# Performance work log

Measured on AMD Instinct MI355X. Metric: run time of the kernel, lower is better.

Reference implementation:

```python
import jax, jax.numpy as jnp
import numpy as np


def setup_inputs() -> dict:
    key = jax.random.key(0)
    k1, k2, k3, k4 = jax.random.split(key, 4)
    B, N, DIN, DOUT = 4, 4096, 512, 64
    x = jax.random.normal(k1, (B, N, DIN), dtype=jnp.float32)
    Wq = jax.random.normal(k2, (DIN, DOUT), dtype=jnp.float32) * (1.0 / np.sqrt(DIN))
    Wk = jax.random.normal(k3, (DIN, DOUT), dtype=jnp.float32) * (1.0 / np.sqrt(DIN))
    Wv = jax.random.normal(k4, (DIN, DOUT), dtype=jnp.float32) * (1.0 / np.sqrt(DIN))
    return {"x": x, "Wq": Wq, "Wk": Wk, "Wv": Wv}


def reference(x, Wq, Wk, Wv):
    # x: [B, N, Din]; projections: [B, N, Dout]
    q = jnp.einsum('bnd,de->bne', x, Wq)
    k = jnp.einsum('bnd,de->bne', x, Wk)
    v = jnp.einsum('bnd,de->bne', x, Wv)
    N = x.shape[1]
    scale = 1.0 / jnp.sqrt(jnp.asarray(k.shape[-1], dtype=x.dtype))
    # scores: [B, N, N]; causal mask (strict upper triangle -> -inf)
    scores = jnp.einsum('bqe,bke->bqk', q, k)
    causal = jnp.tril(jnp.ones((N, N), dtype=bool))  # True where allowed
    scores = jnp.where(causal[None], scores, -jnp.inf)
    att = jax.nn.softmax(scores * scale, axis=-1)
    # dropout p=0.0 -> identity (eval-mode equivalent)
    return jnp.einsum('bqk,bke->bqe', att, v)
```

## Files before the change

kernel.cpp:

```cpp
#include <hip/hip_runtime.h>
#include <hip/hip_bf16.h>

#define BB 4
#define NN 4096
#define DIN 512
#define DD 64

typedef __attribute__((ext_vector_type(8))) short short8;
typedef __attribute__((ext_vector_type(4))) float f32x4;
typedef __attribute__((ext_vector_type(4))) unsigned short us4;
typedef __attribute__((ext_vector_type(2))) unsigned int u32x2;
using bf16 = __hip_bfloat16;

#define QSCALE 0.18033688011112042f

__device__ inline void mfma_16x16x32(f32x4& d, short8 a, short8 b) {
    asm("v_mfma_f32_16x16x32_bf16 %0, %1, %2, %0" : "+v"(d) : "v"(a), "v"(b));
}

__device__ inline unsigned cvt_pk_bf16(float lo, float hi) {
    unsigned r;
    asm("v_cvt_pk_bf16_f32 %0, %1, %2" : "=v"(r) : "v"(lo), "v"(hi));
    return r;
}

__device__ inline short8 load_cvt8(const float* __restrict__ src) {
    f32x4 f0 = *(const f32x4*)(src);
    f32x4 f1 = *(const f32x4*)(src + 4);
    bf16 t[8];
    #pragma unroll
    for (int j = 0; j < 4; ++j) t[j]     = __float2bfloat16(f0[j]);
    #pragma unroll
    for (int j = 0; j < 4; ++j) t[4 + j] = __float2bfloat16(f1[j]);
    return *(short8*)t;
}

__host__ __device__ inline int pfx(int qt, int cl) {
    int K = 2 << cl;
    int n = qt + K;
    int a = n >> (cl + 1);
    int r = n - (a << (cl + 1));
    return a * (a - 1) * (K >> 1) + r * a;
}

__global__ __launch_bounds__(256) void convw_kernel(
    const float* __restrict__ Wq, const float* __restrict__ Wk,
    const float* __restrict__ Wv, bf16* __restrict__ WT)
{
    int idx = blockIdx.x * 256 + threadIdx.x;
    int w   = idx >> 15;
    int rem = idx & 32767;
    int n   = rem >> 9;
    int kk  = rem & 511;
    const float* W = (w == 0) ? Wq : (w == 1) ? Wk : Wv;
    WT[idx] = __float2bfloat16(W[kk * DD + n]);
}

__global__ __launch_bounds__(256) void proj_kernel(
    const float* __restrict__ x, const bf16* __restrict__ WT,
    bf16* __restrict__ q, bf16* __restrict__ k, bf16* __restrict__ vT)
{
    __shared__ __align__(16) char xs[65536];
    const int tid   = threadIdx.x;
    const int row0  = blockIdx.x * 64;
    const int b     = row0 >> 12;
    const int nrow0 = row0 & 4095;

    const float* xb = x + (size_t)row0 * DIN;
    #pragma unroll
    for (int i = 0; i < 16; ++i) {
        int c   = tid + i * 256;
        int row = c >> 6;
        int cc  = c & 63;
        const float* src = xb + row * DIN + cc * 8;
        int off = row * 1024 + ((cc * 16) ^ ((row & 7) << 4));
        *(short8*)(xs + off) = load_cvt8(src);
    }
    __syncthreads();

    const int lane  = tid & 63;
    const int l16   = lane & 15;
    const int lg    = lane >> 4;
    const int wave  = tid >> 6;
    const int cbase = wave * 48;

    f32x4 acc[4][3];
    #pragma unroll
    for (int rt = 0; rt < 4; ++rt)
        #pragma unroll
        for (int ct = 0; ct < 3; ++ct) acc[rt][ct] = (f32x4){0.f, 0.f, 0.f, 0.f};

    const bf16* wb = WT + (size_t)(cbase + l16) * DIN + lg * 8;

    #pragma unroll 2
    for (int ks = 0; ks < 16; ++ks) {
        short8 a[4], bfr[3];
        #pragma unroll
        for (int rt = 0; rt < 4; ++rt) {
            int row = rt * 16 + l16;
            a[rt] = *(const short8*)(xs + row * 1024 +
                                     ((ks * 64 + lg * 16) ^ ((row & 7) << 4)));
        }
        #pragma unroll
        for (int ct = 0; ct < 3; ++ct)
            bfr[ct] = *(const short8*)(wb + ct * 16 * DIN + ks * 32);
        #pragma unroll
        for (int rt = 0; rt < 4; ++rt)
            #pragma unroll
            for (int ct = 0; ct < 3; ++ct)
                mfma_16x16x32(acc[rt][ct], a[rt], bfr[ct]);
    }

    #pragma unroll
    for (int ct = 0; ct < 3; ++ct) {
        int g = cbase + ct * 16 + l16;
        int w = g >> 6;
        int n = g & 63;
        #pragma unroll
        for (int rt = 0; rt < 4; ++rt) {
            if (w == 2) {
                us4 pv;
                #pragma unroll
                for (int r = 0; r < 4; ++r) {
                    bf16 hv = __float2bfloat16(acc[rt][ct][r]);
                    pv[r] = *(unsigned short*)&hv;
                }
                *(us4*)(vT + ((size_t)b * DD + n) * NN + nrow0 + rt * 16 + lg * 4) = pv;
            } else {
                bf16* dst = (w == 0) ? q : k;
                float sc  = (w == 0) ? QSCALE : 1.0f;
                #pragma unroll
                for (int r = 0; r < 4; ++r) {
                    int row = nrow0 + rt * 16 + lg * 4 + r;
                    dst[((size_t)b * NN + row) * DD + n] =
                        __float2bfloat16(acc[rt][ct][r] * sc);
                }
            }
        }
    }
}

__global__ __launch_bounds__(256) void attn_split_kernel(
    const bf16* __restrict__ q, const bf16* __restrict__ k,
    const bf16* __restrict__ vT,
    unsigned short* __restrict__ partO, float* __restrict__ partML,
    float* __restrict__ out, int cl)
{
    const int perB = pfx(64, cl);
    const int wblk = blockIdx.x;
    const int b    = wblk / perB;
    const int u    = wblk - b * perB;
    int lo = 0, hi = 63;
    while (lo < hi) {
        int mid = (lo + hi + 1) >> 1;
        if (pfx(mid, cl) <= u) lo = mid; else hi = mid - 1;
    }
    const int qt = lo;
    const int s  = u - pfx(qt, cl);
    const size_t sidx = (size_t)wblk;

    const int T  = (qt + 2) >> 1;
    const int t0 = s << cl;
    int t1 = t0 + (1 << cl); if (t1 > T) t1 = T;
    const int K2 = 2 << cl;
    const int U  = (qt + K2) >> (cl + 1);

    const int wave = threadIdx.x >> 6;
    const int lane = threadIdx.x & 63;
    const int l16  = lane & 15;
    const int lg   = lane >> 4;

    __shared__ __align__(16) char klds[16384];
    __shared__ __align__(16) char vlds[16384];
    __shared__ __align__(16) char plds[4][4096];
    char* pbl = plds[wave];
    const int swz = (l16 & 7) << 4;

    const int row0g = qt * 64 + wave * 16;
    const int qrow  = row0g + l16;

    const bf16* qbase = q + ((size_t)b * NN + row0g + l16) * DD + lg * 8;
    short8 qfrag0 = *(const short8*)(qbase);
    short8 qfrag1 = *(const short8*)(qbase + 32);

    f32x4 oacc[4];
    #pragma unroll
    for (int dt = 0; dt < 4; ++dt) oacc[dt] = (f32x4){0.f, 0.f, 0.f, 0.f};
    float m = -INFINITY, l = 0.f;

    const char* kglob = (const char*)(k  + (size_t)b * NN * DD);
    const char* vglob = (const char*)(vT + (size_t)b * DD * NN);
    short8 kst[4], vst[4];
    int k_wr[4], v_wr[4], v_dd[4];
    #pragma unroll
    for (int i = 0; i < 4; ++i) {
        int L = wave * 4096 + i * 1024 + lane * 16;
        k_wr[i] = L ^ (((L >> 7) & 7) << 4);
        int dd = wave * 16 + i * 4 + (lane >> 4);
        v_dd[i] = dd;
        v_wr[i] = dd * 256 + (((lane & 15) * 16) ^ ((dd & 7) << 4));
    }

    {
        const char* kt = kglob + (size_t)t0 * 16384;
        const char* vt = vglob + (size_t)t0 * 256;
        #pragma unroll
        for (int i = 0; i < 4; ++i)
            kst[i] = *(const short8*)(kt + wave * 4096 + i * 1024 + lane * 16);
        #pragma unroll
        for (int i = 0; i < 4; ++i)
            vst[i] = *(const short8*)(vt + (size_t)v_dd[i] * 8192 + (lane & 15) * 16);
        #pragma unroll
        for (int i = 0; i < 4; ++i) *(short8*)(klds + k_wr[i]) = kst[i];
        #pragma unroll
        for (int i = 0; i < 4; ++i) *(short8*)(vlds + v_wr[i]) = vst[i];
    }
    __syncthreads();

    #pragma unroll 1
    for (int t = t0; t < t1; ++t) {
        f32x4 sc[8];
        #pragma unroll
        for (int ct = 0; ct < 8; ++ct) sc[ct] = (f32x4){0.f, 0.f, 0.f, 0.f};
        __builtin_amdgcn_s_setprio(1);
        #pragma unroll
        for (int ct = 0; ct < 8; ++ct) {
            short8 kf0 = *(const short8*)(klds + (ct * 16 + l16) * 128 + ((lg * 16) ^ swz));
            short8 kf1 = *(const short8*)(klds + (ct * 16 + l16) * 128 + ((64 + lg * 16) ^ swz));
            mfma_16x16x32(sc[ct], kf0, qfrag0);
            mfma_16x16x32(sc[ct], kf1, qfrag1);
        }
        __builtin_amdgcn_s_setprio(0);

        if (t + 1 < t1) {
            const char* kt = kglob + (size_t)(t + 1) * 16384;
            const char* vt = vglob + (size_t)(t + 1) * 256;
            #pragma unroll
            for (int i = 0; i < 4; ++i)
                kst[i] = *(const short8*)(kt + wave * 4096 + i * 1024 + lane * 16);
            #pragma unroll
            for (int i = 0; i < 4; ++i)
                vst[i] = *(const short8*)(vt + (size_t)v_dd[i] * 8192 + (lane & 15) * 16);
        }

        if (t * 128 + 127 > row0g) {
            #pragma unroll
            for (int ct = 0; ct < 8; ++ct) {
                int gk = t * 128 + ct * 16 + lg * 4;
                #pragma unroll
                for (int r = 0; r < 4; ++r)
                    if (gk + r > qrow)
                        sc[ct][r] = -INFINITY;
            }
        }

        float m4[8];
        #pragma unroll
        for (int ct = 0; ct < 8; ++ct)
            m4[ct] = fmaxf(fmaxf(sc[ct][0], sc[ct][1]), fmaxf(sc[ct][2], sc[ct][3]));
        float mt = fmaxf(fmaxf(fmaxf(m4[0], m4[1]), fmaxf(m4[2], m4[3])),
                         fmaxf(fmaxf(m4[4], m4[5]), fmaxf(m4[6], m4[7])));
        mt = fmaxf(mt, __shfl_xor(mt, 16));
        mt = fmaxf(mt, __shfl_xor(mt, 32));

        float mn    = fmaxf(m, mt);
        float alpha = exp2f(m - mn);
        m = mn;

        float s4[8];
        #pragma unroll
        for (int ct = 0; ct < 8; ++ct) {
            float p0 = exp2f(sc[ct][0] - m);
            float p1 = exp2f(sc[ct][1] - m);
            float p2 = exp2f(sc[ct][2] - m);
            float p3 = exp2f(sc[ct][3] - m);
            sc[ct][0] = p0; sc[ct][1] = p1; sc[ct][2] = p2; sc[ct][3] = p3;
            s4[ct] = (p0 + p1) + (p2 + p3);
        }
        float ls = ((s4[0] + s4[1]) + (s4[2] + s4[3])) +
                   ((s4[4] + s4[5]) + (s4[6] + s4[7]));
        ls += __shfl_xor(ls, 16);
        ls += __shfl_xor(ls, 32);
        l = l * alpha + ls;

        float ar[4];
        #pragma unroll
        for (int r = 0; r < 4; ++r) ar[r] = __shfl(alpha, lg * 4 + r);
        #pragma unroll
        for (int dt = 0; dt < 4; ++dt)
            #pragma unroll
            for (int r = 0; r < 4; ++r)
                oacc[dt][r] *= ar[r];

        #pragma unroll
        for (int ct = 0; ct < 8; ++ct) {
            u32x2 pw = (u32x2){cvt_pk_bf16(sc[ct][0], sc[ct][1]),
                               cvt_pk_bf16(sc[ct][2], sc[ct][3])};
            *(u32x2*)(pbl + l16 * 256 + ((ct * 32 + lg * 8) ^ swz)) = pw;
        }
        asm volatile("s_waitcnt lgkmcnt(0)" ::: "memory");
        short8 pa[4];
        #pragma unroll
        for (int kc = 0; kc < 4; ++kc)
            pa[kc] = *(const short8*)(pbl + l16 * 256 + ((kc * 64 + lg * 16) ^ swz));

        __builtin_amdgcn_s_setprio(1);
        #pragma unroll
        for (int dt = 0; dt < 4; ++dt) {
            #pragma unroll
            for (int kc = 0; kc < 4; ++kc) {
                short8 vf = *(const short8*)(vlds + (dt * 16 + l16) * 256 +
                                             ((kc * 64 + lg * 16) ^ swz));
                mfma_16x16x32(oacc[dt], pa[kc], vf);
            }
        }
        __builtin_amdgcn_s_setprio(0);

        if (t + 1 < t1) {
            __syncthreads();
            #pragma unroll
            for (int i = 0; i < 4; ++i) *(short8*)(klds + k_wr[i]) = kst[i];
            #pragma unroll
            for (int i = 0; i < 4; ++i) *(short8*)(vlds + v_wr[i]) = vst[i];
            __syncthreads();
        }
    }

    if (U == 1) {
        float lr[4];
        #pragma unroll
        for (int r = 0; r < 4; ++r) lr[r] = __shfl(l, lg * 4 + r);
        #pragma unroll
        for (int dt = 0; dt < 4; ++dt) {
            #pragma unroll
            for (int r = 0; r < 4; ++r) {
                int row = row0g + lg * 4 + r;
                out[((size_t)b * NN + row) * DD + dt * 16 + l16] =
                    oacc[dt][r] / lr[r];
            }
        }
        return;
    }

    {
        unsigned short hv[16];
        #pragma unroll
        for (int dt = 0; dt < 4; ++dt)
            #pragma unroll
            for (int r = 0; r < 4; ++r) {
                bf16 h = __float2bfloat16(oacc[dt][r]);
                hv[dt * 4 + r] = *(unsigned short*)&h;
            }
        unsigned short* dst = partO + sidx * 4096 + wave * 1024 + lane * 16;
        *(short8*)(dst)     = *(short8*)(hv);
        *(short8*)(dst + 8) = *(short8*)(hv + 8);
    }
    if (lg == 0) {
        partML[sidx * 128 + wave * 16 + l16]      = m;
        partML[sidx * 128 + 64 + wave * 16 + l16] = l;
    }
}

__global__ __launch_bounds__(256) void combine_kernel(
    const unsigned short* __restrict__ partO, const float* __restrict__ partML,
    float* __restrict__ out, int cl)
{
    const int blk2 = blockIdx.x;
    const int half = blk2 & 1;
    const int blk  = blk2 >> 1;
    const int qt   = blk & 63;
    const int b    = blk >> 6;

    const int K2 = 2 << cl;
    const int U  = (qt + K2) >> (cl + 1);
    if (U == 1) return;

    const int tid  = threadIdx.x;
    const int w    = tid >> 6;
    const int lane = tid & 63;
    const int l16  = lane & 15;
    const int lg   = lane >> 4;

    const int perB = pfx(64, cl);
    const size_t base = (size_t)b * perB + pfx(qt, cl);

    float M[4] = {-INFINITY, -INFINITY, -INFINITY, -INFINITY};
    for (int s = 0; s < U; ++s)
        #pragma unroll
        for (int r = 0; r < 4; ++r)
            M[r] = fmaxf(M[r], partML[(base + s) * 128 + w * 16 + lg * 4 + r]);

    float L[4] = {0.f, 0.f, 0.f, 0.f};
    float acc[8];
    #pragma unroll
    for (int i = 0; i < 8; ++i) acc[i] = 0.f;

    for (int s = 0; s < U; ++s) {
        float e[4];
        #pragma unroll
        for (int r = 0; r < 4; ++r) {
            float ms = partML[(base + s) * 128 + w * 16 + lg * 4 + r];
            e[r] = exp2f(ms - M[r]);
            L[r] += partML[(base + s) * 128 + 64 + w * 16 + lg * 4 + r] * e[r];
        }
        short8 v = *(const short8*)(partO + (base + s) * 4096 + w * 1024 +
                                    lane * 16 + half * 8);
        #pragma unroll
        for (int j = 0; j < 8; ++j) {
            unsigned fb = ((unsigned)(unsigned short)v[j]) << 16;
            acc[j] += *(float*)&fb * e[j & 3];
        }
    }
    #pragma unroll
    for (int j = 0; j < 8; ++j) {
        int reg = half * 8 + j;
        int row = qt * 64 + w * 16 + lg * 4 + (j & 3);
        int dd  = (reg >> 2) * 16 + l16;
        out[((size_t)b * NN + row) * DD + dd] = acc[j] / L[j & 3];
    }
}

extern "C" void kernel_launch(void* const* d_in, const int* in_sizes, int n_in,
                              void* d_out, int out_size, void* d_ws, size_t ws_size,
                              hipStream_t stream) {
    const float* x  = (const float*)d_in[0];
    const float* Wq = (const float*)d_in[1];
    const float* Wk = (const float*)d_in[2];
    const float* Wv = (const float*)d_in[3];

    bf16* q  = (bf16*)d_ws;
    bf16* k  = q  + (size_t)BB * NN * DD;
    bf16* vT = k  + (size_t)BB * NN * DD;
    bf16* WT = vT + (size_t)BB * NN * DD;
    char* pbase = (char*)(WT + 3 * DD * DIN);
    size_t mis = (size_t)pbase & 15;
    if (mis) pbase += 16 - mis;
    size_t fixed = (size_t)(pbase - (char*)d_ws);

    int cl = 2, perB = 0;
    for (; cl <= 3; ++cl) {
        perB = pfx(64, cl);
        size_t need = fixed + (size_t)BB * perB * (128 * 4 + 4096 * 2);
        if (need <= ws_size) break;
    }
    if (cl > 3) { cl = 3; perB = pfx(64, cl); }

    float* partML = (float*)pbase;
    unsigned short* partO = (unsigned short*)(partML + (size_t)BB * perB * 128);

    convw_kernel<<<(3 * DD * DIN) / 256, 256, 0, stream>>>(Wq, Wk, Wv, WT);
    proj_kernel<<<BB * NN / 64, 256, 0, stream>>>(x, WT, q, k, vT);
    attn_split_kernel<<<BB * perB, 256, 0, stream>>>(q, k, vT, partO, partML,
                                                     (float*)d_out, cl);
    combine_kernel<<<BB * 64 * 2, 256, 0, stream>>>(partO, partML, (float*)d_out, cl);
}
```

Before: 57.90 us.

## Halve attention key tile to 64 and rescale split-KV chunking

Shrinks the key/value tile in the split attention kernel from 128 to 64 keys, halving LDS buffers, staging registers and per-tile MFMA work, and rewrites the prefix/split arithmetic to match. The chunk-length exponent default rises from 2 to 3, so each split still spans up to 512 keys. The smaller tile lowers LDS and register use, which could raise occupancy and cuts masked work on diagonal tiles. The cost is twice as many loop iterations, with more barriers and softmax rescale steps per key.

```diff
diff --git a/kernel.cpp b/kernel.cpp
--- a/kernel.cpp
+++ b/kernel.cpp
@@ -36,11 +36,10 @@
 }
 
 __host__ __device__ inline int pfx(int qt, int cl) {
-    int K = 2 << cl;
-    int n = qt + K;
-    int a = n >> (cl + 1);
-    int r = n - (a << (cl + 1));
-    return a * (a - 1) * (K >> 1) + r * a;
+    int C = 1 << cl;
+    int a = qt >> cl;
+    int r = qt & (C - 1);
+    return C * a * (a + 1) / 2 + r * (a + 1);
 }
 
 __global__ __launch_bounds__(256) void convw_kernel(
@@ -159,20 +158,20 @@
     const int s  = u - pfx(qt, cl);
     const size_t sidx = (size_t)wblk;
 
-    const int T  = (qt + 2) >> 1;
+    const int C  = 1 << cl;
+    const int T  = qt + 1;
     const int t0 = s << cl;
-    int t1 = t0 + (1 << cl); if (t1 > T) t1 = T;
-    const int K2 = 2 << cl;
-    const int U  = (qt + K2) >> (cl + 1);
+    int t1 = t0 + C; if (t1 > T) t1 = T;
+    const int U  = (qt + C) >> cl;
 
     const int wave = threadIdx.x >> 6;
     const int lane = threadIdx.x & 63;
     const int l16  = lane & 15;
     const int lg   = lane >> 4;
 
-    __shared__ __align__(16) char klds[16384];
-    __shared__ __align__(16) char vlds[16384];
-    __shared__ __align__(16) char plds[4][4096];
+    __shared__ __align__(16) char klds[8192];
+    __shared__ __align__(16) char vlds[8192];
+    __shared__ __align__(16) char plds[4][2048];
     char* pbl = plds[wave];
     const int swz = (l16 & 7) << 4;
 
@@ -190,41 +189,41 @@
 
     const char* kglob = (const char*)(k  + (size_t)b * NN * DD);
     const char* vglob = (const char*)(vT + (size_t)b * DD * NN);
-    short8 kst[4], vst[4];
-    int k_wr[4], v_wr[4], v_dd[4];
-    #pragma unroll
-    for (int i = 0; i < 4; ++i) {
-        int L = wave * 4096 + i * 1024 + lane * 16;
-        k_wr[i] = L ^ (((L >> 7) & 7) << 4);
-        int dd = wave * 16 + i * 4 + (lane >> 4);
-        v_dd[i] = dd;
-        v_wr[i] = dd * 256 + (((lane & 15) * 16) ^ ((dd & 7) << 4));
+    short8 kst[2], vst[2];
+    int k_src[2], k_wr[2], v_src[2], v_wr[2];
+    #pragma unroll
+    for (int i = 0; i < 2; ++i) {
+        int L = threadIdx.x * 16 + i * 4096;
+        k_src[i] = L;
+        k_wr[i]  = L ^ (((L >> 7) & 7) << 4);
+        int dd    = L >> 7;
+        int inner = L & 127;
+        v_src[i] = dd * 8192 + inner;
+        v_wr[i]  = dd * 128 + (inner ^ ((dd & 7) << 4));
     }
 
     {
-        const char* kt = kglob + (size_t)t0 * 16384;
-        const char* vt = vglob + (size_t)t0 * 256;
-        #pragma unroll
-        for (int i = 0; i < 4; ++i)
-            kst[i] = *(const short8*)(kt + wave * 4096 + i * 1024 + lane * 16);
-        #pragma unroll
-        for (int i = 0; i < 4; ++i)
-            vst[i] = *(const short8*)(vt + (size_t)v_dd[i] * 8192 + (lane & 15) * 16);
-        #pragma unroll
-        for (int i = 0; i < 4; ++i) *(short8*)(klds + k_wr[i]) = kst[i];
-        #pragma unroll
-        for (int i = 0; i < 4; ++i) *(short8*)(vlds + v_wr[i]) = vst[i];
+        const char* kt = kglob + (size_t)t0 * 8192;
+        const char* vt = vglob + (size_t)t0 * 128;
+        #pragma unroll
+        for (int i = 0; i < 2; ++i) kst[i] = *(const short8*)(kt + k_src[i]);
+        #pragma unroll
+        for (int i = 0; i < 2; ++i) vst[i] = *(const short8*)(vt + v_src[i]);
+        #pragma unroll
+        for (int i = 0; i < 2; ++i) *(short8*)(klds + k_wr[i]) = kst[i];
+        #pragma unroll
+        for (int i = 0; i < 2; ++i) *(short8*)(vlds + v_wr[i]) = vst[i];
     }
     __syncthreads();
 
     #pragma unroll 1
     for (int t = t0; t < t1; ++t) {
-        f32x4 sc[8];
-        #pragma unroll
-        for (int ct = 0; ct < 8; ++ct) sc[ct] = (f32x4){0.f, 0.f, 0.f, 0.f};
+        f32x4 sc[4];
+        #pragma unroll
+        for (int ct = 0; ct < 4; ++ct) sc[ct] = (f32x4){0.f, 0.f, 0.f, 0.f};
         __builtin_amdgcn_s_setprio(1);
         #pragma unroll
-        for (int ct = 0; ct < 8; ++ct) {
+        for (int ct = 0; ct < 4; ++ct) {
             short8 kf0 = *(const short8*)(klds + (ct * 16 + l16) * 128 + ((lg * 16) ^ swz));
             short8 kf1 = *(const short8*)(klds + (ct * 16 + l16) * 128 + ((64 + lg * 16) ^ swz));
             mfma_16x16x32(sc[ct], kf0, qfrag0);
@@ -233,20 +232,18 @@
         __builtin_amdgcn_s_setprio(0);
 
         if (t + 1 < t1) {
-            const char* kt = kglob + (size_t)(t + 1) * 16384;
-            const char* vt = vglob + (size_t)(t + 1) * 256;
-            #pragma unroll
-            for (int i = 0; i < 4; ++i)
-                kst[i] = *(const short8*)(kt + wave * 4096 + i * 1024 + lane * 16);
-            #pragma unroll
-            for (int i = 0; i < 4; ++i)
-                vst[i] = *(const short8*)(vt + (size_t)v_dd[i] * 8192 + (lane & 15) * 16);
-        }
-
-        if (t * 128 + 127 > row0g) {
-            #pragma unroll
-            for (int ct = 0; ct < 8; ++ct) {
-                int gk = t * 128 + ct * 16 + lg * 4;
+            const char* kt = kglob + (size_t)(t + 1) * 8192;
+            const char* vt = vglob + (size_t)(t + 1) * 128;
+            #pragma unroll
+            for (int i = 0; i < 2; ++i) kst[i] = *(const short8*)(kt + k_src[i]);
+            #pragma unroll
+            for (int i = 0; i < 2; ++i) vst[i] = *(const short8*)(vt + v_src[i]);
+        }
+
+        if (t * 64 + 63 > row0g) {
+            #pragma unroll
+            for (int ct = 0; ct < 4; ++ct) {
+                int gk = t * 64 + ct * 16 + lg * 4;
                 #pragma unroll
                 for (int r = 0; r < 4; ++r)
                     if (gk + r > qrow)
@@ -254,12 +251,11 @@
             }
         }
 
-        float m4[8];
-        #pragma unroll
-        for (int ct = 0; ct < 8; ++ct)
+        float m4[4];
+        #pragma unroll
+        for (int ct = 0; ct < 4; ++ct)
             m4[ct] = fmaxf(fmaxf(sc[ct][0], sc[ct][1]), fmaxf(sc[ct][2], sc[ct][3]));
-        float mt = fmaxf(fmaxf(fmaxf(m4[0], m4[1]), fmaxf(m4[2], m4[3])),
-                         fmaxf(fmaxf(m4[4], m4[5]), fmaxf(m4[6], m4[7])));
+        float mt = fmaxf(fmaxf(m4[0], m4[1]), fmaxf(m4[2], m4[3]));
         mt = fmaxf(mt, __shfl_xor(mt, 16));
         mt = fmaxf(mt, __shfl_xor(mt, 32));
 
@@ -267,9 +263,9 @@
         float alpha = exp2f(m - mn);
         m = mn;
 
-        float s4[8];
-        #pragma unroll
-        for (int ct = 0; ct < 8; ++ct) {
+        float s4[4];
+        #pragma unroll
+        for (int ct = 0; ct < 4; ++ct) {
             float p0 = exp2f(sc[ct][0] - m);
             float p1 = exp2f(sc[ct][1] - m);
             float p2 = exp2f(sc[ct][2] - m);
@@ -277,8 +273,7 @@
             sc[ct][0] = p0; sc[ct][1] = p1; sc[ct][2] = p2; sc[ct][3] = p3;
             s4[ct] = (p0 + p1) + (p2 + p3);
         }
-        float ls = ((s4[0] + s4[1]) + (s4[2] + s4[3])) +
-                   ((s4[4] + s4[5]) + (s4[6] + s4[7]));
+        float ls = (s4[0] + s4[1]) + (s4[2] + s4[3]);
         ls += __shfl_xor(ls, 16);
         ls += __shfl_xor(ls, 32);
         l = l * alpha + ls;
@@ -293,35 +288,33 @@
                 oacc[dt][r] *= ar[r];
 
         #pragma unroll
-        for (int ct = 0; ct < 8; ++ct) {
+        for (int ct = 0; ct < 4; ++ct) {
             u32x2 pw = (u32x2){cvt_pk_bf16(sc[ct][0], sc[ct][1]),
                                cvt_pk_bf16(sc[ct][2], sc[ct][3])};
-            *(u32x2*)(pbl + l16 * 256 + ((ct * 32 + lg * 8) ^ swz)) = pw;
+            *(u32x2*)(pbl + l16 * 128 + ((ct * 32 + lg * 8) ^ swz)) = pw;
         }
         asm volatile("s_waitcnt lgkmcnt(0)" ::: "memory");
-        short8 pa[4];
-        #pragma unroll
-        for (int kc = 0; kc < 4; ++kc)
-            pa[kc] = *(const short8*)(pbl + l16 * 256 + ((kc * 64 + lg * 16) ^ swz));
+        short8 pa[2];
+        #pragma unroll
+        for (int kc = 0; kc < 2; ++kc)
+            pa[kc] = *(const short8*)(pbl + l16 * 128 + ((kc * 64 + lg * 16) ^ swz));
 
         __builtin_amdgcn_s_setprio(1);
         #pragma unroll
         for (int dt = 0; dt < 4; ++dt) {
-            #pragma unroll
-            for (int kc = 0; kc < 4; ++kc) {
-                short8 vf = *(const short8*)(vlds + (dt * 16 + l16) * 256 +
-                                             ((kc * 64 + lg * 16) ^ swz));
-                mfma_16x16x32(oacc[dt], pa[kc], vf);
-            }
+            short8 vf0 = *(const short8*)(vlds + (dt * 16 + l16) * 128 + ((lg * 16) ^ swz));
+            short8 vf1 = *(const short8*)(vlds + (dt * 16 + l16) * 128 + ((64 + lg * 16) ^ swz));
+            mfma_16x16x32(oacc[dt], pa[0], vf0);
+            mfma_16x16x32(oacc[dt], pa[1], vf1);
         }
         __builtin_amdgcn_s_setprio(0);
 
         if (t + 1 < t1) {
             __syncthreads();
             #pragma unroll
-            for (int i = 0; i < 4; ++i) *(short8*)(klds + k_wr[i]) = kst[i];
-            #pragma unroll
-            for (int i = 0; i < 4; ++i) *(short8*)(vlds + v_wr[i]) = vst[i];
+            for (int i = 0; i < 2; ++i) *(short8*)(klds + k_wr[i]) = kst[i];
+            #pragma unroll
+            for (int i = 0; i < 2; ++i) *(short8*)(vlds + v_wr[i]) = vst[i];
             __syncthreads();
         }
     }
@@ -371,8 +364,8 @@
     const int qt   = blk & 63;
     const int b    = blk >> 6;
 
-    const int K2 = 2 << cl;
-    const int U  = (qt + K2) >> (cl + 1);
+    const int C = 1 << cl;
+    const int U = (qt + C) >> cl;
     if (U == 1) return;
 
     const int tid  = threadIdx.x;
@@ -437,13 +430,13 @@
     if (mis) pbase += 16 - mis;
     size_t fixed = (size_t)(pbase - (char*)d_ws);
 
-    int cl = 2, perB = 0;
-    for (; cl <= 3; ++cl) {
+    int cl = 3, perB = 0;
+    for (; cl <= 4; ++cl) {
         perB = pfx(64, cl);
         size_t need = fixed + (size_t)BB * perB * (128 * 4 + 4096 * 2);
         if (need <= ws_size) break;
     }
-    if (cl > 3) { cl = 3; perB = pfx(64, cl); }
+    if (cl > 4) { cl = 4; perB = pfx(64, cl); }
 
     float* partML = (float*)pbase;
     unsigned short* partO = (unsigned short*)(partML + (size_t)BB * perB * 128);
```

Result: slower. 59.52 us (+2.8%).
